# Performance work log

Hardware: AMD Instinct MI355X
Metric: run time of the kernel (lower is better)

## Reference

```python
import jax, jax.numpy as jnp
import numpy as np

B, S, H = 32, 2048, 1024
UNITS = 1024


def setup_inputs() -> dict:
    key = jax.random.key(0)
    ks = jax.random.split(key, 8)
    scale_h = 1.0 / np.sqrt(H)
    scale_u = 1.0 / np.sqrt(UNITS)
    return {
        "query": jax.random.normal(ks[0], (B, H), dtype=jnp.float32),
        "values": jax.random.normal(ks[1], (B, S, H), dtype=jnp.float32),
        "W1": jax.random.normal(ks[2], (H, UNITS), dtype=jnp.float32) * scale_h,
        "b1": jnp.zeros((UNITS,), dtype=jnp.float32),
        "W2": jax.random.normal(ks[3], (H, UNITS), dtype=jnp.float32) * scale_h,
        "b2": jnp.zeros((UNITS,), dtype=jnp.float32),
        "V": jax.random.normal(ks[4], (UNITS, 1), dtype=jnp.float32) * scale_u,
        "bv": jnp.zeros((1,), dtype=jnp.float32),
    }


def reference(query, values, W1, b1, W2, b2, V, bv):
    # proj_v: [B, S, units]; proj_q: [B, 1, units] (query expanded on time axis)
    proj_v = jnp.einsum("bsh,hu->bsu", values, W1) + b1
    proj_q = (query @ W2 + b2)[:, None, :]
    # score: [B, S, 1]
    score = jnp.tanh(proj_v + proj_q) @ V + bv
    attention_weights = jax.nn.softmax(score, axis=1)  # softmax over seq axis
    context_vector = jnp.sum(attention_weights * values, axis=1)  # [B, H]
    return context_vector, attention_weights
```

## Files before the change

kernel.cpp:

```cpp
#include <hip/hip_runtime.h>

#define H 1024
#define UNITS 1024
#define BATCH 32
#define SEQ 2048
#define M_TOT (BATCH * SEQ)

typedef __attribute__((ext_vector_type(8))) short bf16x8;
typedef __attribute__((ext_vector_type(8))) unsigned short u16x8;
typedef __attribute__((ext_vector_type(4))) float f32x4;

__device__ __forceinline__ unsigned short f2bf(float f) {
  union { float f; unsigned u; } x; x.f = f;
  unsigned r = x.u + 0x7FFFu + ((x.u >> 16) & 1u);
  return (unsigned short)(r >> 16);
}
__device__ __forceinline__ float bf2f(unsigned short h) {
  union { unsigned u; float f; } x; x.u = (unsigned)h << 16;
  return x.f;
}

__device__ __forceinline__ void gll16(const unsigned short* g, unsigned short* l) {
  __builtin_amdgcn_global_load_lds(
      (const __attribute__((address_space(1))) void*)g,
      (__attribute__((address_space(3))) void*)l, 16, 0, 0);
}

__global__ void k_prep(const float* __restrict__ values, unsigned short* __restrict__ Vb,
                       const float* __restrict__ W1, unsigned short* __restrict__ W1T,
                       const float* __restrict__ query, const float* __restrict__ W2,
                       const float* __restrict__ b2, float* __restrict__ projq,
                       float* __restrict__ scores, float* __restrict__ ctx) {
  __shared__ float sh[1056];
  const int blk = blockIdx.x;
  const int tid = threadIdx.x;
  if (blk < 2048) {
    for (int u = blk; u < 32768; u += 2048) {
      size_t i = ((size_t)u * 256 + tid) * 8;
      float4 v0 = *reinterpret_cast<const float4*>(values + i);
      float4 v1 = *reinterpret_cast<const float4*>(values + i + 4);
      union { unsigned short h[8]; u16x8 v; } p;
      p.h[0] = f2bf(v0.x); p.h[1] = f2bf(v0.y); p.h[2] = f2bf(v0.z); p.h[3] = f2bf(v0.w);
      p.h[4] = f2bf(v1.x); p.h[5] = f2bf(v1.y); p.h[6] = f2bf(v1.z); p.h[7] = f2bf(v1.w);
      *reinterpret_cast<u16x8*>(Vb + i) = p.v;
    }
  } else if (blk < 3072) {
    float (*tile)[33] = reinterpret_cast<float(*)[33]>(sh);
    const int t = blk - 2048;
    const int bx = t & 31, by = t >> 5;
    const int tx = tid & 31, ty = tid >> 5;
#pragma unroll
    for (int i = 0; i < 4; ++i)
      tile[ty + i * 8][tx] = W1[(by * 32 + ty + i * 8) * UNITS + bx * 32 + tx];
    __syncthreads();
#pragma unroll
    for (int i = 0; i < 4; ++i)
      W1T[(bx * 32 + ty + i * 8) * H + by * 32 + tx] = f2bf(tile[tx][ty + i * 8]);
  } else if (blk < 3200) {
    float* q = sh;
    const int t = blk - 3072;
    const int b = t >> 2;
    const int u = (t & 3) * 256 + tid;
    for (int i = tid; i < H; i += 256) q[i] = query[b * H + i];
    __syncthreads();
    float acc = 0.f;
#pragma unroll 8
    for (int k = 0; k < H; ++k) acc = fmaf(q[k], W2[k * UNITS + u], acc);
    projq[b * UNITS + u] = acc + b2[u];
  } else {
    const int idx = (blk - 3200) * 256 + tid;
    float4 z = make_float4(0.f, 0.f, 0.f, 0.f);
    *reinterpret_cast<float4*>(scores + idx * 8) = z;
    *reinterpret_cast<float4*>(scores + idx * 8 + 4) = z;
    *reinterpret_cast<float4*>(ctx + idx * 4) = z;
  }
}

#define BM 256
#define BN 256
#define NKT 32

__global__ __launch_bounds__(512, 2) void k_score3(
    const unsigned short* __restrict__ Vb,
    const unsigned short* __restrict__ W1T,
    const float* __restrict__ b1,
    const float* __restrict__ projq,
    const float* __restrict__ V,
    float* __restrict__ scores)
{
  __shared__ unsigned short As[4][128][64];
  __shared__ unsigned short Bs[4][128][64];

  const int tid = threadIdx.x;
  const int lane = tid & 63;
  const int wave = tid >> 6;
  const int wm = wave >> 2;
  const int wn = wave & 3;
  const int li = lane & 15, hi = lane >> 4;
  const int lr2 = li >> 1;
  const int pcol = (((((li & 1) << 2) + hi) ^ lr2) & 7) << 3;

  const int g = blockIdx.x;
  const int xcd = g & 7;
  const int local = g >> 3;
  const int n_t = local & 3;
  const int m_t = xcd + ((local >> 2) << 3);
  const int m0 = m_t * BM;
  const int n0 = n_t * BN;

  const int sL = (lane & 7) ^ (lane >> 3);
  const int srow = 2 * (lane >> 3) + (sL >> 2);
  const int scol = (sL & 3) << 3;

  auto STAGE_A = [&](int bf, int kt) {
#pragma unroll
    for (int q = 0; q < 2; ++q) {
      int mb = wave * 32 + q * 16;
      gll16(&Vb[(size_t)(m0 + mb + srow) * H + kt * 32 + scol],
            &As[bf][wave * 16 + q * 8][0]);
    }
  };
  auto STAGE_B = [&](int bf, int kt) {
#pragma unroll
    for (int q = 0; q < 2; ++q) {
      int mb = wave * 32 + q * 16;
      gll16(&W1T[(size_t)(n0 + mb + srow) * H + kt * 32 + scol],
            &Bs[bf][wave * 16 + q * 8][0]);
    }
  };

  f32x4 acc[8][4] = {};

  STAGE_A(0, 0); STAGE_B(0, 0);
  STAGE_A(1, 1); STAGE_B(1, 1);
  STAGE_A(2, 2); STAGE_B(2, 2);

#pragma unroll 4
  for (int c = 0; c < NKT; ++c) {
    const int buf = c & 3;
    const int nbuf = (c + 3) & 3;
    const int cn = (c < NKT - 3) ? c + 3 : NKT - 1;

    asm volatile("s_waitcnt vmcnt(8)" ::: "memory");
    __builtin_amdgcn_s_barrier();

    bf16x8 a[8], b[4];
#pragma unroll
    for (int i = 0; i < 8; ++i)
      a[i] = *reinterpret_cast<const bf16x8*>(&As[buf][wm * 64 + i * 8 + lr2][pcol]);
    STAGE_A(nbuf, cn);
#pragma unroll
    for (int j = 0; j < 4; ++j)
      b[j] = *reinterpret_cast<const bf16x8*>(&Bs[buf][wn * 32 + j * 8 + lr2][pcol]);
    STAGE_B(nbuf, cn);

#pragma unroll
    for (int i = 0; i < 8; ++i)
#pragma unroll
      for (int j = 0; j < 4; ++j)
        acc[i][j] = __builtin_amdgcn_mfma_f32_16x16x32_bf16(a[i], b[j], acc[i][j], 0, 0, 0);
  }

  const int b = m0 >> 11;
  float bias[4], vv[4];
#pragma unroll
  for (int j = 0; j < 4; ++j) {
    int u = n0 + wn * 64 + j * 16 + li;
    bias[j] = b1[u] + projq[b * UNITS + u];
    vv[j] = V[u];
  }
#pragma unroll
  for (int mi = 0; mi < 8; ++mi) {
#pragma unroll
    for (int r = 0; r < 4; ++r) {
      float s = 0.f;
#pragma unroll
      for (int j = 0; j < 4; ++j) {
        float x = acc[mi][j][r] + bias[j];
        float e = __expf(2.f * x);
        s += (1.f - 2.f / (e + 1.f)) * vv[j];
      }
      s += __shfl_xor(s, 1);
      s += __shfl_xor(s, 2);
      s += __shfl_xor(s, 4);
      s += __shfl_xor(s, 8);
      if (li == 0) {
        int row = m0 + wm * 128 + mi * 16 + hi * 4 + r;
        atomicAdd(&scores[row], s);
      }
    }
  }
}

__global__ void k_transpose_w1(const float* __restrict__ W1, unsigned short* __restrict__ W1T) {
  __shared__ float tile[32][33];
  int bx = blockIdx.x, by = blockIdx.y;
  int tx = threadIdx.x, ty = threadIdx.y;
#pragma unroll
  for (int i = 0; i < 4; ++i)
    tile[ty + i * 8][tx] = W1[(by * 32 + ty + i * 8) * UNITS + bx * 32 + tx];
  __syncthreads();
#pragma unroll
  for (int i = 0; i < 4; ++i)
    W1T[(bx * 32 + ty + i * 8) * H + by * 32 + tx] = f2bf(tile[tx][ty + i * 8]);
}

__global__ void k_projq(const float* __restrict__ query, const float* __restrict__ W2,
                        const float* __restrict__ b2, float* __restrict__ projq) {
  __shared__ float q[H];
  int b = blockIdx.x;
  int u = blockIdx.y * 256 + threadIdx.x;
  for (int i = threadIdx.x; i < H; i += 256) q[i] = query[b * H + i];
  __syncthreads();
  float acc = 0.f;
#pragma unroll 8
  for (int k = 0; k < H; ++k) acc = fmaf(q[k], W2[k * UNITS + u], acc);
  projq[b * UNITS + u] = acc + b2[u];
}

#define FBM 128
#define FBN 128
#define FBK 64
#define LDK 72
__global__ __launch_bounds__(256) void k_score_f32(
    const float* __restrict__ values, const unsigned short* __restrict__ W1T,
    const float* __restrict__ b1, const float* __restrict__ projq,
    const float* __restrict__ V, float* __restrict__ scores)
{
  __shared__ unsigned short Asf[FBM][LDK];
  __shared__ unsigned short Bsf[FBN][LDK];
  const int tid = threadIdx.x;
  const int lane = tid & 63;
  const int wave = tid >> 6;
  const int wm = wave >> 1, wn = wave & 1;
  const int li = lane & 15, hi = lane >> 4;
  const int n0 = blockIdx.x * FBN;
  const int m0 = blockIdx.y * FBM;
  f32x4 acc[4][4] = {};
  for (int k0 = 0; k0 < H; k0 += FBK) {
    __syncthreads();
#pragma unroll
    for (int q = 0; q < 8; ++q) {
      int idx = q * 256 + tid;
      int row = idx >> 4;
      int kc = (idx & 15) << 2;
      float4 v = *reinterpret_cast<const float4*>(&values[(size_t)(m0 + row) * H + k0 + kc]);
      union { unsigned short h[4]; unsigned long long u64; } p;
      p.h[0] = f2bf(v.x); p.h[1] = f2bf(v.y); p.h[2] = f2bf(v.z); p.h[3] = f2bf(v.w);
      *reinterpret_cast<unsigned long long*>(&Asf[row][kc]) = p.u64;
    }
#pragma unroll
    for (int q = 0; q < 4; ++q) {
      int idx = q * 256 + tid;
      int row = idx >> 3;
      int kc = (idx & 7) << 3;
      *reinterpret_cast<u16x8*>(&Bsf[row][kc]) =
          *reinterpret_cast<const u16x8*>(&W1T[(size_t)(n0 + row) * H + k0 + kc]);
    }
    __syncthreads();
#pragma unroll
    for (int ks = 0; ks < 2; ++ks) {
      const int kofs = ks * 32 + 8 * hi;
      bf16x8 a[4], bb[4];
#pragma unroll
      for (int i = 0; i < 4; ++i)
        a[i] = *reinterpret_cast<const bf16x8*>(&Asf[wm * 64 + i * 16 + li][kofs]);
#pragma unroll
      for (int i = 0; i < 4; ++i)
        bb[i] = *reinterpret_cast<const bf16x8*>(&Bsf[wn * 64 + i * 16 + li][kofs]);
#pragma unroll
      for (int mi = 0; mi < 4; ++mi)
#pragma unroll
        for (int ni = 0; ni < 4; ++ni)
          acc[mi][ni] = __builtin_amdgcn_mfma_f32_16x16x32_bf16(a[mi], bb[ni], acc[mi][ni], 0, 0, 0);
    }
  }
  const int b = m0 >> 11;
  float bias[4], vv[4];
#pragma unroll
  for (int ni = 0; ni < 4; ++ni) {
    int u = n0 + wn * 64 + ni * 16 + li;
    bias[ni] = b1[u] + projq[b * UNITS + u];
    vv[ni] = V[u];
  }
#pragma unroll
  for (int mi = 0; mi < 4; ++mi) {
#pragma unroll
    for (int r = 0; r < 4; ++r) {
      float s = 0.f;
#pragma unroll
      for (int ni = 0; ni < 4; ++ni) {
        float x = acc[mi][ni][r] + bias[ni];
        float e = __expf(2.f * x);
        s += (1.f - 2.f / (e + 1.f)) * vv[ni];
      }
      s += __shfl_xor(s, 1);
      s += __shfl_xor(s, 2);
      s += __shfl_xor(s, 4);
      s += __shfl_xor(s, 8);
      if (li == 0) atomicAdd(&scores[m0 + wm * 64 + mi * 16 + hi * 4 + r], s);
    }
  }
}

__global__ void k_softmax(const float* __restrict__ scores, float* __restrict__ wts) {
  __shared__ float red[8];
  int b = blockIdx.x;
  int t = threadIdx.x;
  float v[8];
  float mx = -3.4e38f;
#pragma unroll
  for (int i = 0; i < 8; ++i) {
    v[i] = scores[b * SEQ + i * 256 + t];
    mx = fmaxf(mx, v[i]);
  }
#pragma unroll
  for (int o = 1; o < 64; o <<= 1) mx = fmaxf(mx, __shfl_xor(mx, o));
  if ((t & 63) == 0) red[t >> 6] = mx;
  __syncthreads();
  mx = fmaxf(fmaxf(red[0], red[1]), fmaxf(red[2], red[3]));
  float sum = 0.f;
#pragma unroll
  for (int i = 0; i < 8; ++i) { v[i] = __expf(v[i] - mx); sum += v[i]; }
#pragma unroll
  for (int o = 1; o < 64; o <<= 1) sum += __shfl_xor(sum, o);
  if ((t & 63) == 0) red[4 + (t >> 6)] = sum;
  __syncthreads();
  float inv = 1.f / (red[4] + red[5] + red[6] + red[7]);
#pragma unroll
  for (int i = 0; i < 8; ++i) wts[b * SEQ + i * 256 + t] = v[i] * inv;
}

__global__ void k_context_bf(const unsigned short* __restrict__ Vb,
                             const float* __restrict__ wts, float* __restrict__ ctx) {
  int b = blockIdx.x, sc = blockIdx.y;
  int h4 = threadIdx.x * 4;
  const unsigned short* vb = Vb + (size_t)b * SEQ * H;
  float a0 = 0, a1 = 0, a2 = 0, a3 = 0;
  int s0 = sc * 64;
#pragma unroll 4
  for (int s = s0; s < s0 + 64; ++s) {
    float w = wts[b * SEQ + s];
    ushort4 v = *reinterpret_cast<const ushort4*>(&vb[(size_t)s * H + h4]);
    a0 = fmaf(w, bf2f(v.x), a0);
    a1 = fmaf(w, bf2f(v.y), a1);
    a2 = fmaf(w, bf2f(v.z), a2);
    a3 = fmaf(w, bf2f(v.w), a3);
  }
  atomicAdd(&ctx[b * H + h4 + 0], a0);
  atomicAdd(&ctx[b * H + h4 + 1], a1);
  atomicAdd(&ctx[b * H + h4 + 2], a2);
  atomicAdd(&ctx[b * H + h4 + 3], a3);
}

__global__ void k_context(const float* __restrict__ values, const float* __restrict__ wts,
                          float* __restrict__ ctx) {
  int b = blockIdx.x, hc = blockIdx.y, sc = blockIdx.z;
  int h = hc * 256 + threadIdx.x;
  const float* vb = values + (size_t)b * SEQ * H;
  float acc = 0.f;
  int s0 = sc * 128;
#pragma unroll 4
  for (int s = s0; s < s0 + 128; ++s)
    acc = fmaf(wts[b * SEQ + s], vb[(size_t)s * H + h], acc);
  atomicAdd(&ctx[b * H + h], acc);
}

extern "C" void kernel_launch(void* const* d_in, const int* in_sizes, int n_in,
                              void* d_out, int out_size, void* d_ws, size_t ws_size,
                              hipStream_t stream) {
  (void)in_sizes; (void)n_in; (void)out_size;
  const float* query  = (const float*)d_in[0];
  const float* values = (const float*)d_in[1];
  const float* W1     = (const float*)d_in[2];
  const float* b1     = (const float*)d_in[3];
  const float* W2     = (const float*)d_in[4];
  const float* b2     = (const float*)d_in[5];
  const float* V      = (const float*)d_in[6];

  float* out = (float*)d_out;
  float* ctx = out;
  float* wts = out + BATCH * H;

  const size_t vb_bytes = (size_t)M_TOT * H * 2;
  const size_t need = vb_bytes + (2u << 20) + (256u << 10) + (128u << 10);

  if (ws_size >= need) {
    char* ws = (char*)d_ws;
    unsigned short* Vb  = (unsigned short*)ws;
    unsigned short* W1T = (unsigned short*)(ws + vb_bytes);
    float* scores = (float*)(ws + vb_bytes + (2u << 20));
    float* projq  = (float*)(ws + vb_bytes + (2u << 20) + (256u << 10));

    k_prep<<<3232, 256, 0, stream>>>(values, Vb, W1, W1T, query, W2, b2, projq,
                                     scores, ctx);
    k_score3<<<(M_TOT / BM) * (UNITS / BN), 512, 0, stream>>>(Vb, W1T, b1, projq, V, scores);
    k_softmax<<<BATCH, 256, 0, stream>>>(scores, wts);
    k_context_bf<<<dim3(BATCH, 32), 256, 0, stream>>>(Vb, wts, ctx);
  } else {
    char* ws = (char*)d_ws;
    unsigned short* W1T = (unsigned short*)ws;
    float* scores = (float*)(ws + (2u << 20));
    float* projq  = (float*)(ws + (2u << 20) + (256u << 10));

    hipMemsetAsync(scores, 0, M_TOT * sizeof(float), stream);
    hipMemsetAsync(ctx, 0, BATCH * H * sizeof(float), stream);

    k_transpose_w1<<<dim3(32, 32), dim3(32, 8), 0, stream>>>(W1, W1T);
    k_projq<<<dim3(32, 4), 256, 0, stream>>>(query, W2, b2, projq);
    k_score_f32<<<dim3(UNITS / FBN, M_TOT / FBM), 256, 0, stream>>>(values, W1T, b1, projq, V, scores);
    k_softmax<<<BATCH, 256, 0, stream>>>(scores, wts);
    k_context<<<dim3(BATCH, H / 256, 16), 256, 0, stream>>>(values, wts, ctx);
  }
}
```

Measured before the change: 324.7 us.

## Fuse fp32-to-bf16 conversion of values into the GEMM A-tile loader

```diff
diff --git a/kernel.cpp b/kernel.cpp
--- a/kernel.cpp
+++ b/kernel.cpp
@@ -15,10 +15,6 @@
   unsigned r = x.u + 0x7FFFu + ((x.u >> 16) & 1u);
   return (unsigned short)(r >> 16);
 }
-__device__ __forceinline__ float bf2f(unsigned short h) {
-  union { unsigned u; float f; } x; x.u = (unsigned)h << 16;
-  return x.f;
-}
 
 __device__ __forceinline__ void gll16(const unsigned short* g, unsigned short* l) {
   __builtin_amdgcn_global_load_lds(
@@ -26,28 +22,16 @@
       (__attribute__((address_space(3))) void*)l, 16, 0, 0);
 }
 
-__global__ void k_prep(const float* __restrict__ values, unsigned short* __restrict__ Vb,
-                       const float* __restrict__ W1, unsigned short* __restrict__ W1T,
-                       const float* __restrict__ query, const float* __restrict__ W2,
-                       const float* __restrict__ b2, float* __restrict__ projq,
-                       float* __restrict__ scores, float* __restrict__ ctx) {
+__global__ void k_prep2(const float* __restrict__ W1, unsigned short* __restrict__ W1T,
+                        const float* __restrict__ query, const float* __restrict__ W2,
+                        const float* __restrict__ b2, float* __restrict__ projq,
+                        float* __restrict__ scores, float* __restrict__ ctx) {
   __shared__ float sh[1056];
   const int blk = blockIdx.x;
   const int tid = threadIdx.x;
-  if (blk < 2048) {
-    for (int u = blk; u < 32768; u += 2048) {
-      size_t i = ((size_t)u * 256 + tid) * 8;
-      float4 v0 = *reinterpret_cast<const float4*>(values + i);
-      float4 v1 = *reinterpret_cast<const float4*>(values + i + 4);
-      union { unsigned short h[8]; u16x8 v; } p;
-      p.h[0] = f2bf(v0.x); p.h[1] = f2bf(v0.y); p.h[2] = f2bf(v0.z); p.h[3] = f2bf(v0.w);
-      p.h[4] = f2bf(v1.x); p.h[5] = f2bf(v1.y); p.h[6] = f2bf(v1.z); p.h[7] = f2bf(v1.w);
-      *reinterpret_cast<u16x8*>(Vb + i) = p.v;
-    }
-  } else if (blk < 3072) {
+  if (blk < 1024) {
     float (*tile)[33] = reinterpret_cast<float(*)[33]>(sh);
-    const int t = blk - 2048;
-    const int bx = t & 31, by = t >> 5;
+    const int bx = blk & 31, by = blk >> 5;
     const int tx = tid & 31, ty = tid >> 5;
 #pragma unroll
     for (int i = 0; i < 4; ++i)
@@ -56,9 +40,9 @@
 #pragma unroll
     for (int i = 0; i < 4; ++i)
       W1T[(bx * 32 + ty + i * 8) * H + by * 32 + tx] = f2bf(tile[tx][ty + i * 8]);
-  } else if (blk < 3200) {
+  } else if (blk < 1152) {
     float* q = sh;
-    const int t = blk - 3072;
+    const int t = blk - 1024;
     const int b = t >> 2;
     const int u = (t & 3) * 256 + tid;
     for (int i = tid; i < H; i += 256) q[i] = query[b * H + i];
@@ -68,7 +52,7 @@
     for (int k = 0; k < H; ++k) acc = fmaf(q[k], W2[k * UNITS + u], acc);
     projq[b * UNITS + u] = acc + b2[u];
   } else {
-    const int idx = (blk - 3200) * 256 + tid;
+    const int idx = (blk - 1152) * 256 + tid;
     float4 z = make_float4(0.f, 0.f, 0.f, 0.f);
     *reinterpret_cast<float4*>(scores + idx * 8) = z;
     *reinterpret_cast<float4*>(scores + idx * 8 + 4) = z;
@@ -80,15 +64,15 @@
 #define BN 256
 #define NKT 32
 
-__global__ __launch_bounds__(512, 2) void k_score3(
-    const unsigned short* __restrict__ Vb,
+__global__ __launch_bounds__(512, 2) void k_score4(
+    const float* __restrict__ values,
     const unsigned short* __restrict__ W1T,
     const float* __restrict__ b1,
     const float* __restrict__ projq,
     const float* __restrict__ V,
     float* __restrict__ scores)
 {
-  __shared__ unsigned short As[4][128][64];
+  __shared__ unsigned short As[2][128][64];
   __shared__ unsigned short Bs[4][128][64];
 
   const int tid = threadIdx.x;
@@ -112,14 +96,10 @@
   const int srow = 2 * (lane >> 3) + (sL >> 2);
   const int scol = (sL & 3) << 3;
 
-  auto STAGE_A = [&](int bf, int kt) {
-#pragma unroll
-    for (int q = 0; q < 2; ++q) {
-      int mb = wave * 32 + q * 16;
-      gll16(&Vb[(size_t)(m0 + mb + srow) * H + kt * 32 + scol],
-            &As[bf][wave * 16 + q * 8][0]);
-    }
-  };
+  const float* vA = values + (size_t)(m0 + wave * 32 + srow) * H + scol;
+  const int arow = wave * 16 + (lane >> 3);
+  const int acol = (lane & 7) << 3;
+
   auto STAGE_B = [&](int bf, int kt) {
 #pragma unroll
     for (int q = 0; q < 2; ++q) {
@@ -128,37 +108,65 @@
             &Bs[bf][wave * 16 + q * 8][0]);
     }
   };
+  auto LOAD_A = [&](int kt, float4* r) {
+    const float* p0 = vA + kt * 32;
+    const float* p1 = p0 + (size_t)16 * H;
+    r[0] = *reinterpret_cast<const float4*>(p0);
+    r[1] = *reinterpret_cast<const float4*>(p0 + 4);
+    r[2] = *reinterpret_cast<const float4*>(p1);
+    r[3] = *reinterpret_cast<const float4*>(p1 + 4);
+  };
+  auto CVTW = [&](int ab, const float4* r) {
+    union { unsigned short h[8]; u16x8 v; } p0, p1;
+    p0.h[0] = f2bf(r[0].x); p0.h[1] = f2bf(r[0].y);
+    p0.h[2] = f2bf(r[0].z); p0.h[3] = f2bf(r[0].w);
+    p0.h[4] = f2bf(r[1].x); p0.h[5] = f2bf(r[1].y);
+    p0.h[6] = f2bf(r[1].z); p0.h[7] = f2bf(r[1].w);
+    p1.h[0] = f2bf(r[2].x); p1.h[1] = f2bf(r[2].y);
+    p1.h[2] = f2bf(r[2].z); p1.h[3] = f2bf(r[2].w);
+    p1.h[4] = f2bf(r[3].x); p1.h[5] = f2bf(r[3].y);
+    p1.h[6] = f2bf(r[3].z); p1.h[7] = f2bf(r[3].w);
+    *reinterpret_cast<u16x8*>(&As[ab][arow][acol]) = p0.v;
+    *reinterpret_cast<u16x8*>(&As[ab][arow + 8][acol]) = p1.v;
+  };
 
   f32x4 acc[8][4] = {};
-
-  STAGE_A(0, 0); STAGE_B(0, 0);
-  STAGE_A(1, 1); STAGE_B(1, 1);
-  STAGE_A(2, 2); STAGE_B(2, 2);
-
-#pragma unroll 4
-  for (int c = 0; c < NKT; ++c) {
-    const int buf = c & 3;
-    const int nbuf = (c + 3) & 3;
-    const int cn = (c < NKT - 3) ? c + 3 : NKT - 1;
-
-    asm volatile("s_waitcnt vmcnt(8)" ::: "memory");
-    __builtin_amdgcn_s_barrier();
-
+  float4 fA[4], fB[4];
+
+  LOAD_A(0, fA);
+  STAGE_B(0, 0); STAGE_B(1, 1); STAGE_B(2, 2);
+  asm volatile("s_waitcnt vmcnt(6)" ::: "memory");
+  CVTW(0, fA);
+  LOAD_A(1, fB);
+  asm volatile("s_waitcnt vmcnt(8)" ::: "memory");
+  asm volatile("s_waitcnt lgkmcnt(0)" ::: "memory");
+  __builtin_amdgcn_s_barrier();
+
+  auto TILE = [&](int c, float4* fCvt, float4* fLoad) {
     bf16x8 a[8], b[4];
 #pragma unroll
     for (int i = 0; i < 8; ++i)
-      a[i] = *reinterpret_cast<const bf16x8*>(&As[buf][wm * 64 + i * 8 + lr2][pcol]);
-    STAGE_A(nbuf, cn);
+      a[i] = *reinterpret_cast<const bf16x8*>(&As[c & 1][wm * 64 + i * 8 + lr2][pcol]);
 #pragma unroll
     for (int j = 0; j < 4; ++j)
-      b[j] = *reinterpret_cast<const bf16x8*>(&Bs[buf][wn * 32 + j * 8 + lr2][pcol]);
-    STAGE_B(nbuf, cn);
-
+      b[j] = *reinterpret_cast<const bf16x8*>(&Bs[c & 3][wn * 32 + j * 8 + lr2][pcol]);
+    STAGE_B((c + 3) & 3, (c + 3 < NKT) ? c + 3 : NKT - 1);
+    asm volatile("s_waitcnt vmcnt(2)" ::: "memory");
+    CVTW((c + 1) & 1, fCvt);
+    LOAD_A((c + 2 < NKT) ? c + 2 : NKT - 1, fLoad);
 #pragma unroll
     for (int i = 0; i < 8; ++i)
 #pragma unroll
       for (int j = 0; j < 4; ++j)
         acc[i][j] = __builtin_amdgcn_mfma_f32_16x16x32_bf16(a[i], b[j], acc[i][j], 0, 0, 0);
+    asm volatile("s_waitcnt lgkmcnt(0)" ::: "memory");
+    __builtin_amdgcn_s_barrier();
+  };
+
+#pragma unroll 2
+  for (int c = 0; c < NKT; c += 2) {
+    TILE(c, fB, fA);
+    TILE(c + 1, fA, fB);
   }
 
   const int b = m0 >> 11;
@@ -331,21 +339,21 @@
   for (int i = 0; i < 8; ++i) wts[b * SEQ + i * 256 + t] = v[i] * inv;
 }
 
-__global__ void k_context_bf(const unsigned short* __restrict__ Vb,
-                             const float* __restrict__ wts, float* __restrict__ ctx) {
+__global__ void k_context_f32v(const float* __restrict__ values,
+                               const float* __restrict__ wts, float* __restrict__ ctx) {
   int b = blockIdx.x, sc = blockIdx.y;
   int h4 = threadIdx.x * 4;
-  const unsigned short* vb = Vb + (size_t)b * SEQ * H;
+  const float* vb = values + (size_t)b * SEQ * H;
   float a0 = 0, a1 = 0, a2 = 0, a3 = 0;
   int s0 = sc * 64;
 #pragma unroll 4
   for (int s = s0; s < s0 + 64; ++s) {
     float w = wts[b * SEQ + s];
-    ushort4 v = *reinterpret_cast<const ushort4*>(&vb[(size_t)s * H + h4]);
-    a0 = fmaf(w, bf2f(v.x), a0);
-    a1 = fmaf(w, bf2f(v.y), a1);
-    a2 = fmaf(w, bf2f(v.z), a2);
-    a3 = fmaf(w, bf2f(v.w), a3);
+    float4 v = *reinterpret_cast<const float4*>(&vb[(size_t)s * H + h4]);
+    a0 = fmaf(w, v.x, a0);
+    a1 = fmaf(w, v.y, a1);
+    a2 = fmaf(w, v.z, a2);
+    a3 = fmaf(w, v.w, a3);
   }
   atomicAdd(&ctx[b * H + h4 + 0], a0);
   atomicAdd(&ctx[b * H + h4 + 1], a1);
@@ -382,21 +390,18 @@
   float* ctx = out;
   float* wts = out + BATCH * H;
 
-  const size_t vb_bytes = (size_t)M_TOT * H * 2;
-  const size_t need = vb_bytes + (2u << 20) + (256u << 10) + (128u << 10);
+  const size_t need = (2u << 20) + (256u << 10) + (128u << 10);
 
   if (ws_size >= need) {
     char* ws = (char*)d_ws;
-    unsigned short* Vb  = (unsigned short*)ws;
-    unsigned short* W1T = (unsigned short*)(ws + vb_bytes);
-    float* scores = (float*)(ws + vb_bytes + (2u << 20));
-    float* projq  = (float*)(ws + vb_bytes + (2u << 20) + (256u << 10));
-
-    k_prep<<<3232, 256, 0, stream>>>(values, Vb, W1, W1T, query, W2, b2, projq,
-                                     scores, ctx);
-    k_score3<<<(M_TOT / BM) * (UNITS / BN), 512, 0, stream>>>(Vb, W1T, b1, projq, V, scores);
+    unsigned short* W1T = (unsigned short*)ws;
+    float* scores = (float*)(ws + (2u << 20));
+    float* projq  = (float*)(ws + (2u << 20) + (256u << 10));
+
+    k_prep2<<<1184, 256, 0, stream>>>(W1, W1T, query, W2, b2, projq, scores, ctx);
+    k_score4<<<(M_TOT / BM) * (UNITS / BN), 512, 0, stream>>>(values, W1T, b1, projq, V, scores);
     k_softmax<<<BATCH, 256, 0, stream>>>(scores, wts);
-    k_context_bf<<<dim3(BATCH, 32), 256, 0, stream>>>(Vb, wts, ctx);
+    k_context_f32v<<<dim3(BATCH, 32), 256, 0, stream>>>(values, wts, ctx);
   } else {
     char* ws = (char*)d_ws;
     unsigned short* W1T = (unsigned short*)ws;
```

Measured after the change: 316.9 us. -2.4%, faster.
